# Kernel tuning notes

Measured on AMD Instinct MI355X. Metric: run time of the kernel, lower is better.

## Reference

```python
import jax, jax.numpy as jnp
import numpy as np

B, C, H, W = 4, 256, 64, 64
CQK = C // 2


def setup_inputs() -> dict:
    key = jax.random.key(0)
    ks = jax.random.split(key, 8)
    s = 0.05
    return {
        "x": jax.random.normal(ks[0], (B, C, H, W), dtype=jnp.float32),
        "wq": jax.random.normal(ks[1], (CQK, C), dtype=jnp.float32) * s,
        "bq": jax.random.normal(ks[2], (CQK,), dtype=jnp.float32) * s,
        "wk": jax.random.normal(ks[3], (CQK, C), dtype=jnp.float32) * s,
        "bk": jax.random.normal(ks[4], (CQK,), dtype=jnp.float32) * s,
        "wv": jax.random.normal(ks[5], (C, C), dtype=jnp.float32) * s,
        "bv": jax.random.normal(ks[6], (C,), dtype=jnp.float32) * s,
        "gamma": jax.random.normal(ks[7], (1,), dtype=jnp.float32),
    }


def reference(x, wq, bq, wk, bk, wv, bv, gamma):
    b, c, h, w = x.shape
    n = h * w
    xf = x.reshape(b, c, n)  # [B,C,N]
    # 1x1 convs == per-pixel linear projections
    q = jnp.einsum("oc,bcn->bon", wq, xf) + bq[:, None]  # [B,C/2,N]
    k = jnp.einsum("oc,bcn->bon", wk, xf) + bk[:, None]  # [B,C/2,N]
    v = jnp.einsum("oc,bcn->bon", wv, xf) + bv[:, None]  # [B,C,N]
    # attention[b,m,n'] = softmax_n'( sum_d q[b,d,m] * k[b,d,n'] )
    scores = jnp.einsum("bdm,bdn->bmn", q, k)  # [B,N,N]
    attn = jax.nn.softmax(scores, axis=2)
    # out_feat[b,c,j] = sum_i v[b,c,i] * attn[b,i,j]  (matmul(value, attention))
    af = jnp.einsum("bci,bij->bcj", v, attn)  # [B,C,N]
    out = gamma[0] * af.reshape(b, c, h, w) + x
    return out
```

## Files before the change

kernel.cpp:

```cpp
#include <hip/hip_runtime.h>
#include <hip/hip_bf16.h>


typedef _Float16 f16;
typedef _Float16 f16x4v __attribute__((ext_vector_type(4)));
typedef _Float16 f16x8v __attribute__((ext_vector_type(8)));
typedef float f32x4v __attribute__((ext_vector_type(4)));

static __device__ __forceinline__ f32x4v mfma16(f16x8v a, f16x8v b, f32x4v c) {
  return __builtin_amdgcn_mfma_f32_16x16x32_f16(a, b, c, 0, 0, 0);
}

__global__ void k_wcvt(const float* __restrict__ wq, const float* __restrict__ bq,
                       const float* __restrict__ wk, const float* __restrict__ bk,
                       const float* __restrict__ wv, const float* __restrict__ bv,
                       f16* __restrict__ wh, float* __restrict__ bcat) {
  int o = blockIdx.x;
  int c = threadIdx.x;
  const float* wrow; float bias;
  if (o < 128)      { wrow = wq + (size_t)o * 256;         bias = bq[o]; }
  else if (o < 256) { wrow = wk + (size_t)(o - 128) * 256; bias = bk[o - 128]; }
  else              { wrow = wv + (size_t)(o - 256) * 256; bias = bv[o - 256]; }
  wh[(size_t)(o >> 4) * 4096 + (size_t)(c >> 5) * 512 +
     (size_t)((c >> 3) & 3) * 128 + (o & 15) * 8 + (c & 7)] = (f16)wrow[c];
  if (c == 0) bcat[o] = bias;
}

__global__ void k_xsplit(const float* __restrict__ x, f16* __restrict__ xh) {
  __shared__ float t[64][65];
  int b = blockIdx.z, c0 = blockIdx.y * 64, n0 = blockIdx.x * 64;
  int tx = threadIdx.x & 63, ty = threadIdx.x >> 6;
  const float* xb = x + ((size_t)b * 256 + c0) * 4096 + n0;
#pragma unroll
  for (int r = ty; r < 64; r += 4) t[r][tx] = xb[(size_t)r * 4096 + tx];
  __syncthreads();
  f16* xbb = xh + (size_t)b * 1048576;
#pragma unroll
  for (int k2 = 0; k2 < 2; k2++) {
    int id = k2 * 256 + threadIdx.x;
    int tok = id & 63, oct = id >> 6;
    int tt = n0 + tok;
    f16x8v v;
#pragma unroll
    for (int e = 0; e < 8; e++) v[e] = (f16)t[oct * 8 + e][tok];
    size_t addr = (size_t)(tt >> 4) * 4096 +
                  (size_t)((c0 >> 5) + (oct >> 2)) * 512 +
                  (size_t)(oct & 3) * 128 + (tt & 15) * 8;
    *(f16x8v*)&xbb[addr] = v;
  }
}

__global__ void __launch_bounds__(512, 1)
k_proj(const f16* __restrict__ xh, const f16* __restrict__ wh,
       const float* __restrict__ bcat, f16* __restrict__ qT,
       f16* __restrict__ kT, f16* __restrict__ vT) {
  int ob = blockIdx.x, th = blockIdx.y, b = blockIdx.z;
  int tid = threadIdx.x, l = tid & 63, w = tid >> 6;
  int col = l & 15, quad = l >> 4;
  int tt = w & 3, oh = w >> 2;
  int OT0 = ob * 4 + oh * 2;
  const f16* wtb = wh + (size_t)OT0 * 4096 + l * 8;
  f16x8v wb[2][8];
#pragma unroll
  for (int jt = 0; jt < 2; jt++)
#pragma unroll
    for (int ks = 0; ks < 8; ks++)
      wb[jt][ks] = *(const f16x8v*)(wtb + jt * 4096 + ks * 512);
  float bias0 = bcat[OT0 * 16 + col];
  float bias1 = bcat[OT0 * 16 + 16 + col];
  const f16* atb = xh + (size_t)b * 1048576 + (size_t)(th * 32 + tt) * 4096 + l * 8;
  f16x8v afA[8], afB[8];
#pragma unroll
  for (int ks = 0; ks < 8; ks++) afA[ks] = *(const f16x8v*)(atb + ks * 512);

#define PROJ_BODY(IT, AF, AN, PREF)                                            \
  {                                                                            \
    if (PREF) {                                                                \
      _Pragma("unroll") for (int ks = 0; ks < 8; ks++)                         \
        AN[ks] = *(const f16x8v*)(atb + (size_t)((IT) + 1) * 16384 + ks * 512);\
    }                                                                          \
    f32x4v s0 = {}, s1 = {};                                                   \
    _Pragma("unroll") for (int ks = 0; ks < 8; ks++) {                         \
      s0 = mfma16(AF[ks], wb[0][ks], s0);                                      \
      s1 = mfma16(AF[ks], wb[1][ks], s1);                                      \
    }                                                                          \
    int T = th * 32 + (IT) * 4 + tt;                                           \
    if (ob < 4) {                                                              \
      f16* dst = (ob < 2) ? qT : kT;                                           \
      _Pragma("unroll") for (int jt = 0; jt < 2; jt++) {                       \
        int o = OT0 * 16 + jt * 16 + col;                                      \
        int d = o & 127;                                                       \
        float bs = jt ? bias1 : bias0;                                         \
        size_t base = (size_t)b * 524288 + (size_t)T * 2048 +                  \
                      (size_t)(d >> 5) * 512 + (size_t)((d >> 3) & 3) * 128 +  \
                      (d & 7);                                                 \
        float sv0 = jt ? s1[0] : s0[0], sv1 = jt ? s1[1] : s0[1];              \
        float sv2 = jt ? s1[2] : s0[2], sv3 = jt ? s1[3] : s0[3];              \
        dst[base + (quad * 4 + 0) * 8] = (f16)(sv0 + bs);                      \
        dst[base + (quad * 4 + 1) * 8] = (f16)(sv1 + bs);                      \
        dst[base + (quad * 4 + 2) * 8] = (f16)(sv2 + bs);                      \
        dst[base + (quad * 4 + 3) * 8] = (f16)(sv3 + bs);                      \
      }                                                                        \
    } else {                                                                   \
      int i0 = T * 16 + quad * 4;                                              \
      size_t ibase = (size_t)b * 1048576 + (size_t)(i0 >> 5) * 512 +           \
                     (size_t)((i0 >> 3) & 3) * 128 + (i0 & 7);                 \
      _Pragma("unroll") for (int jt = 0; jt < 2; jt++) {                       \
        int c = OT0 * 16 + jt * 16 + col - 256;                                \
        float bs = jt ? bias1 : bias0;                                         \
        f16x4v pv;                                                             \
        _Pragma("unroll") for (int rg = 0; rg < 4; rg++)                       \
          pv[rg] = (f16)((jt ? s1[rg] : s0[rg]) + bs);                         \
        *(f16x4v*)&vT[ibase + (size_t)(c >> 4) * 65536 + (c & 15) * 8] = pv;   \
      }                                                                        \
    }                                                                          \
  }

  for (int itp = 0; itp < 4; itp++) {
    int itA = itp * 2;
    PROJ_BODY(itA, afA, afB, true)
    PROJ_BODY(itA + 1, afB, afA, itp < 3)
  }
#undef PROJ_BODY
}

__global__ void __launch_bounds__(512, 2)
k_rows(const f16* __restrict__ qT, const f16* __restrict__ kT,
       float* __restrict__ partial) {
  int jblk = blockIdx.x, ih = blockIdx.y, b = blockIdx.z;
  int tid = threadIdx.x, l = tid & 63, w = tid >> 6;
  int col = l & 15;
  int ti = w & 3, jh = w >> 2;
  const f16* ktb = kT + (size_t)b * 524288 + (size_t)(jblk * 8 + jh * 4) * 2048 + l * 8;
  const f16* qtb = qT + (size_t)b * 524288 + (size_t)ti * 2048 + l * 8;
  f16x8v ka[4][4];
#pragma unroll
  for (int jt = 0; jt < 4; jt++)
#pragma unroll
    for (int ks = 0; ks < 4; ks++)
      ka[jt][ks] = *(const f16x8v*)(ktb + jt * 2048 + ks * 512);
  float* pout = partial + ((size_t)(b * 32 + jblk) * 2 + jh) * 4096 + ti * 16 + col;
  int it0 = ih * 16;
  f16x8v qfA[4], qfB[4];
#pragma unroll
  for (int ks = 0; ks < 4; ks++)
    qfA[ks] = *(const f16x8v*)(qtb + (size_t)it0 * 8192 + ks * 512);

#define ROWS_BODY(IT, QF, QN, PREF)                                           \
  {                                                                           \
    if (PREF) {                                                               \
      _Pragma("unroll") for (int ks = 0; ks < 4; ks++)                        \
        QN[ks] = *(const f16x8v*)(qtb + (size_t)((IT) + 1) * 8192 + ks * 512);\
    }                                                                         \
    f32x4v s[4] = {};                                                         \
    _Pragma("unroll") for (int ks = 0; ks < 4; ks++) {                        \
      s[0] = mfma16(ka[0][ks], QF[ks], s[0]);                                 \
      s[1] = mfma16(ka[1][ks], QF[ks], s[1]);                                 \
      s[2] = mfma16(ka[2][ks], QF[ks], s[2]);                                 \
      s[3] = mfma16(ka[3][ks], QF[ks], s[3]);                                 \
    }                                                                         \
    float t = 0.f;                                                            \
    _Pragma("unroll") for (int jt = 0; jt < 4; jt++)                          \
      _Pragma("unroll") for (int rg = 0; rg < 4; rg++)                        \
        t += __expf(s[jt][rg]);                                               \
    t += __shfl_xor(t, 16);                                                   \
    t += __shfl_xor(t, 32);                                                   \
    if (l < 16) pout[(size_t)(IT) * 64] = t;                                  \
  }

  for (int itp = 0; itp < 8; itp++) {
    int itA = it0 + itp * 2;
    ROWS_BODY(itA, qfA, qfB, true)
    ROWS_BODY(itA + 1, qfB, qfA, itp < 7)
  }
#undef ROWS_BODY
}

__global__ void k_rsum(const float* __restrict__ partial, float* __restrict__ rinv) {
  int b = blockIdx.y;
  int i = blockIdx.x * 256 + threadIdx.x;
  const float* p = partial + (size_t)b * 64 * 4096 + i;
  float s = 0.f;
#pragma unroll 8
  for (int jb = 0; jb < 64; jb++) s += p[(size_t)jb * 4096];
  rinv[(size_t)b * 4096 + i] = 1.0f / s;
}

__global__ void __launch_bounds__(512, 1)
k_fav(const f16* __restrict__ qT, const f16* __restrict__ kT,
      const f16* __restrict__ vT, const float* __restrict__ rinv,
      const float* __restrict__ x, const float* __restrict__ gamma,
      float* __restrict__ out) {
  __shared__ f16 sE[2][2][4096];
  int wg = blockIdx.x;
  int lg = (wg & 7) * 32 + (wg >> 3);
  int b = lg >> 6, j0 = (lg & 63) * 64;
  int tid = threadIdx.x, l = tid & 63, w = tid >> 6;
  int col = l & 15, quad = l >> 4;
  int ti = w & 3, tjb = (w >> 2) * 2;
  const f16* ktb = kT + (size_t)b * 524288 + (size_t)(j0 / 16 + tjb) * 2048 + l * 8;
  const f16* qtb = qT + (size_t)b * 524288 + (size_t)ti * 2048 + l * 8;
  const f16* vtb = vT + (size_t)b * 1048576 + (size_t)(w * 2) * 65536 + l * 8;
  const float* rp = rinv + (size_t)b * 4096 + ti * 16 + col;
  f16x8v ka0[4], ka1[4];
#pragma unroll
  for (int ks = 0; ks < 4; ks++) {
    ka0[ks] = *(const f16x8v*)(ktb + ks * 512);
    ka1[ks] = *(const f16x8v*)(ktb + 2048 + ks * 512);
  }
  f16x8v qfA[4], qfB[4], vfA[2][2], vfB[2][2];
  float rvA, rvB;
#pragma unroll
  for (int ks = 0; ks < 4; ks++) {
    qfA[ks] = *(const f16x8v*)(qtb + ks * 512);
    qfB[ks] = *(const f16x8v*)(qtb + 8192 + ks * 512);
  }
  rvA = rp[0];
  rvB = rp[64];
  f32x4v acc[2][4] = {};
  int ig = ti * 2 + (col >> 3);
  int i_lo = col & 7;

#define FAV_QK(QF, RV, SEP, SET)                                               \
  {                                                                            \
    f32x4v s0 = {}, s1 = {};                                                   \
    _Pragma("unroll") for (int ks = 0; ks < 4; ks++) {                         \
      s0 = mfma16(ka0[ks], QF[ks], s0);                                        \
      s1 = mfma16(ka1[ks], QF[ks], s1);                                        \
    }                                                                          \
    _Pragma("unroll") for (int rg = 0; rg < 4; rg++) {                         \
      int jl0 = tjb * 16 + quad * 4 + rg;                                      \
      sE[SEP][SET][jl0 * 64 + ((ig ^ (jl0 & 7)) * 8) + i_lo] =                 \
          (f16)(__expf(s0[rg]) * RV);                                          \
      sE[SEP][SET][(jl0 + 16) * 64 + ((ig ^ (jl0 & 7)) * 8) + i_lo] =          \
          (f16)(__expf(s1[rg]) * RV);                                          \
    }                                                                          \
  }

#define FAV_AV(VF, SEP, SET)                                                   \
  {                                                                            \
    _Pragma("unroll") for (int ks = 0; ks < 2; ks++) {                         \
      int sw = ((ks * 4 + quad) ^ (col & 7)) * 8;                              \
      f16x8v e0 = *(const f16x8v*)&sE[SEP][SET][col * 64 + sw];                \
      f16x8v e1 = *(const f16x8v*)&sE[SEP][SET][(16 + col) * 64 + sw];         \
      f16x8v e2 = *(const f16x8v*)&sE[SEP][SET][(32 + col) * 64 + sw];         \
      f16x8v e3 = *(const f16x8v*)&sE[SEP][SET][(48 + col) * 64 + sw];         \
      acc[0][0] = mfma16(VF[0][ks], e0, acc[0][0]);                            \
      acc[0][1] = mfma16(VF[0][ks], e1, acc[0][1]);                            \
      acc[0][2] = mfma16(VF[0][ks], e2, acc[0][2]);                            \
      acc[0][3] = mfma16(VF[0][ks], e3, acc[0][3]);                            \
      acc[1][0] = mfma16(VF[1][ks], e0, acc[1][0]);                            \
      acc[1][1] = mfma16(VF[1][ks], e1, acc[1][1]);                            \
      acc[1][2] = mfma16(VF[1][ks], e2, acc[1][2]);                            \
      acc[1][3] = mfma16(VF[1][ks], e3, acc[1][3]);                            \
    }                                                                          \
  }

  for (int s = 0; s < 32; s++) {
    int t0 = s * 2;
    int p = s & 1;
#pragma unroll
    for (int mt = 0; mt < 2; mt++)
#pragma unroll
      for (int ks = 0; ks < 2; ks++) {
        vfA[mt][ks] = *(const f16x8v*)(vtb + mt * 65536 + (size_t)(t0 * 2 + ks) * 512);
        vfB[mt][ks] = *(const f16x8v*)(vtb + mt * 65536 + (size_t)(t0 * 2 + 2 + ks) * 512);
      }
    if (p) { FAV_QK(qfA, rvA, 1, 0) FAV_QK(qfB, rvB, 1, 1) }
    else   { FAV_QK(qfA, rvA, 0, 0) FAV_QK(qfB, rvB, 0, 1) }
    asm volatile("s_waitcnt lgkmcnt(0)\n\ts_barrier" ::: "memory");
    if (s < 31) {
#pragma unroll
      for (int ks = 0; ks < 4; ks++) {
        qfA[ks] = *(const f16x8v*)(qtb + (size_t)(t0 + 2) * 8192 + ks * 512);
        qfB[ks] = *(const f16x8v*)(qtb + (size_t)(t0 + 3) * 8192 + ks * 512);
      }
      rvA = rp[(size_t)(t0 + 2) * 64];
      rvB = rp[(size_t)(t0 + 3) * 64];
    }
    if (p) { FAV_AV(vfA, 1, 0) FAV_AV(vfB, 1, 1) }
    else   { FAV_AV(vfA, 0, 0) FAV_AV(vfB, 0, 1) }
  }
#undef FAV_QK
#undef FAV_AV

  float gm = gamma[0];
  const float* xb = x + (size_t)b * 256 * 4096;
  float* ob = out + (size_t)b * 256 * 4096;
#pragma unroll
  for (int mt = 0; mt < 2; mt++)
#pragma unroll
    for (int jt = 0; jt < 4; jt++) {
      int c = w * 32 + mt * 16 + quad * 4;
      int j = j0 + jt * 16 + col;
#pragma unroll
      for (int rg = 0; rg < 4; rg++) {
        size_t off = (size_t)(c + rg) * 4096 + j;
        ob[off] = gm * acc[mt][jt][rg] + xb[off];
      }
    }
}

extern "C" void kernel_launch(void* const* d_in, const int* in_sizes, int n_in,
                              void* d_out, int out_size, void* d_ws, size_t ws_size,
                              hipStream_t stream) {
  (void)in_sizes; (void)n_in; (void)out_size; (void)ws_size;
  const float* x  = (const float*)d_in[0];
  const float* wq = (const float*)d_in[1];
  const float* bq = (const float*)d_in[2];
  const float* wk = (const float*)d_in[3];
  const float* bk = (const float*)d_in[4];
  const float* wv = (const float*)d_in[5];
  const float* bv = (const float*)d_in[6];
  const float* gm = (const float*)d_in[7];
  float* out = (float*)d_out;

  char* ws = (char*)d_ws;
  f16*  xh = (f16*)ws;
  f16*  qT = (f16*)(ws + 8388608);
  f16*  kT = (f16*)(ws + 12582912);
  f16*  vT = (f16*)(ws + 16777216);
  f16*  wh = (f16*)(ws + 25165824);
  float* bcat    = (float*)(ws + 25427968);
  float* rinv    = (float*)(ws + 25430016);
  float* partial = (float*)(ws + 25495552);

  hipLaunchKernelGGL(k_wcvt, dim3(512), dim3(256), 0, stream, wq, bq, wk, bk, wv, bv, wh, bcat);
  hipLaunchKernelGGL(k_xsplit, dim3(64, 4, 4), dim3(256), 0, stream, x, xh);
  hipLaunchKernelGGL(k_proj, dim3(8, 8, 4), dim3(512), 0, stream, xh, wh, bcat, qT, kT, vT);
  hipLaunchKernelGGL(k_rows, dim3(32, 4, 4), dim3(512), 0, stream, qT, kT, partial);
  hipLaunchKernelGGL(k_rsum, dim3(16, 4), dim3(256), 0, stream, partial, rinv);
  hipLaunchKernelGGL(k_fav, dim3(256), dim3(512), 0, stream, qT, kT, vT, rinv, x, gm, out);
}
```

Measured before the change: 180.9 us.

## Merge weight conversion into x split, halve row-sum grid, restructure fav QK split

Folds the weight/bias conversion kernel into the x transpose kernel, removing one launch. The row-sum kernel now processes twice as many query rows per block with half the grid, so each block's register-resident K fragments are reused over more rows. In the fused attention kernel, each wave now computes all four 16-column key tiles for one query tile rather than two key tiles for two query tiles. This cuts per-iteration Q loads and holds more K fragments in registers, at the cost of higher register pressure and a different mix of MFMA and LDS-write work.

```diff
diff --git a/kernel.cpp b/kernel.cpp
--- a/kernel.cpp
+++ b/kernel.cpp
@@ -11,22 +11,22 @@
   return __builtin_amdgcn_mfma_f32_16x16x32_f16(a, b, c, 0, 0, 0);
 }
 
-__global__ void k_wcvt(const float* __restrict__ wq, const float* __restrict__ bq,
-                       const float* __restrict__ wk, const float* __restrict__ bk,
-                       const float* __restrict__ wv, const float* __restrict__ bv,
-                       f16* __restrict__ wh, float* __restrict__ bcat) {
-  int o = blockIdx.x;
-  int c = threadIdx.x;
-  const float* wrow; float bias;
-  if (o < 128)      { wrow = wq + (size_t)o * 256;         bias = bq[o]; }
-  else if (o < 256) { wrow = wk + (size_t)(o - 128) * 256; bias = bk[o - 128]; }
-  else              { wrow = wv + (size_t)(o - 256) * 256; bias = bv[o - 256]; }
-  wh[(size_t)(o >> 4) * 4096 + (size_t)(c >> 5) * 512 +
-     (size_t)((c >> 3) & 3) * 128 + (o & 15) * 8 + (c & 7)] = (f16)wrow[c];
-  if (c == 0) bcat[o] = bias;
-}
-
-__global__ void k_xsplit(const float* __restrict__ x, f16* __restrict__ xh) {
+__global__ void k_xsplit(const float* __restrict__ x, f16* __restrict__ xh,
+                         const float* __restrict__ wq, const float* __restrict__ bq,
+                         const float* __restrict__ wk, const float* __restrict__ bk,
+                         const float* __restrict__ wv, const float* __restrict__ bv,
+                         f16* __restrict__ wh, float* __restrict__ bcat) {
+  int id = blockIdx.x + 64 * (blockIdx.y + 4 * blockIdx.z);
+  if (id < 512) {
+    int o = id, c = threadIdx.x;
+    const float* wrow; float bias;
+    if (o < 128)      { wrow = wq + (size_t)o * 256;         bias = bq[o]; }
+    else if (o < 256) { wrow = wk + (size_t)(o - 128) * 256; bias = bk[o - 128]; }
+    else              { wrow = wv + (size_t)(o - 256) * 256; bias = bv[o - 256]; }
+    wh[(size_t)(o >> 4) * 4096 + (size_t)(c >> 5) * 512 +
+       (size_t)((c >> 3) & 3) * 128 + (o & 15) * 8 + (c & 7)] = (f16)wrow[c];
+    if (c == 0) bcat[o] = bias;
+  }
   __shared__ float t[64][65];
   int b = blockIdx.z, c0 = blockIdx.y * 64, n0 = blockIdx.x * 64;
   int tx = threadIdx.x & 63, ty = threadIdx.x >> 6;
@@ -37,8 +37,8 @@
   f16* xbb = xh + (size_t)b * 1048576;
 #pragma unroll
   for (int k2 = 0; k2 < 2; k2++) {
-    int id = k2 * 256 + threadIdx.x;
-    int tok = id & 63, oct = id >> 6;
+    int id2 = k2 * 256 + threadIdx.x;
+    int tok = id2 & 63, oct = id2 >> 6;
     int tt = n0 + tok;
     f16x8v v;
 #pragma unroll
@@ -140,7 +140,7 @@
     for (int ks = 0; ks < 4; ks++)
       ka[jt][ks] = *(const f16x8v*)(ktb + jt * 2048 + ks * 512);
   float* pout = partial + ((size_t)(b * 32 + jblk) * 2 + jh) * 4096 + ti * 16 + col;
-  int it0 = ih * 16;
+  int it0 = ih * 32;
   f16x8v qfA[4], qfB[4];
 #pragma unroll
   for (int ks = 0; ks < 4; ks++)
@@ -168,10 +168,10 @@
     if (l < 16) pout[(size_t)(IT) * 64] = t;                                  \
   }
 
-  for (int itp = 0; itp < 8; itp++) {
+  for (int itp = 0; itp < 16; itp++) {
     int itA = it0 + itp * 2;
     ROWS_BODY(itA, qfA, qfB, true)
-    ROWS_BODY(itA + 1, qfB, qfA, itp < 7)
+    ROWS_BODY(itA + 1, qfB, qfA, itp < 15)
   }
 #undef ROWS_BODY
 }
@@ -197,54 +197,41 @@
   int b = lg >> 6, j0 = (lg & 63) * 64;
   int tid = threadIdx.x, l = tid & 63, w = tid >> 6;
   int col = l & 15, quad = l >> 4;
-  int ti = w & 3, tjb = (w >> 2) * 2;
-  const f16* ktb = kT + (size_t)b * 524288 + (size_t)(j0 / 16 + tjb) * 2048 + l * 8;
+  int ti = w & 3, sel = w >> 2;
+  const f16* ktb = kT + (size_t)b * 524288 + (size_t)(j0 / 16) * 2048 + l * 8;
   const f16* qtb = qT + (size_t)b * 524288 + (size_t)ti * 2048 + l * 8;
   const f16* vtb = vT + (size_t)b * 1048576 + (size_t)(w * 2) * 65536 + l * 8;
   const float* rp = rinv + (size_t)b * 4096 + ti * 16 + col;
-  f16x8v ka0[4], ka1[4];
-#pragma unroll
-  for (int ks = 0; ks < 4; ks++) {
-    ka0[ks] = *(const f16x8v*)(ktb + ks * 512);
-    ka1[ks] = *(const f16x8v*)(ktb + 2048 + ks * 512);
-  }
-  f16x8v qfA[4], qfB[4], vfA[2][2], vfB[2][2];
-  float rvA, rvB;
-#pragma unroll
-  for (int ks = 0; ks < 4; ks++) {
-    qfA[ks] = *(const f16x8v*)(qtb + ks * 512);
-    qfB[ks] = *(const f16x8v*)(qtb + 8192 + ks * 512);
-  }
-  rvA = rp[0];
-  rvB = rp[64];
+  f16x8v ka[4][4];
+#pragma unroll
+  for (int jt = 0; jt < 4; jt++)
+#pragma unroll
+    for (int ks = 0; ks < 4; ks++)
+      ka[jt][ks] = *(const f16x8v*)(ktb + jt * 2048 + ks * 512);
+  f16x8v qf[4], vfA[2][2], vfB[2][2];
+#pragma unroll
+  for (int ks = 0; ks < 4; ks++)
+    qf[ks] = *(const f16x8v*)(qtb + (size_t)sel * 8192 + ks * 512);
+  float rv = rp[sel * 64];
   f32x4v acc[2][4] = {};
   int ig = ti * 2 + (col >> 3);
   int i_lo = col & 7;
 
-#define FAV_QK(QF, RV, SEP, SET)                                               \
-  {                                                                            \
-    f32x4v s0 = {}, s1 = {};                                                   \
-    _Pragma("unroll") for (int ks = 0; ks < 4; ks++) {                         \
-      s0 = mfma16(ka0[ks], QF[ks], s0);                                        \
-      s1 = mfma16(ka1[ks], QF[ks], s1);                                        \
-    }                                                                          \
-    _Pragma("unroll") for (int rg = 0; rg < 4; rg++) {                         \
-      int jl0 = tjb * 16 + quad * 4 + rg;                                      \
-      sE[SEP][SET][jl0 * 64 + ((ig ^ (jl0 & 7)) * 8) + i_lo] =                 \
-          (f16)(__expf(s0[rg]) * RV);                                          \
-      sE[SEP][SET][(jl0 + 16) * 64 + ((ig ^ (jl0 & 7)) * 8) + i_lo] =          \
-          (f16)(__expf(s1[rg]) * RV);                                          \
-    }                                                                          \
-  }
-
-#define FAV_AV(VF, SEP, SET)                                                   \
+#define FAV_WR(SJ, JT, P)                                                      \
+  _Pragma("unroll") for (int rg = 0; rg < 4; rg++) {                           \
+    int jl = (JT) * 16 + quad * 4 + rg;                                        \
+    sE[P][sel][jl * 64 + ((ig ^ (jl & 7)) * 8) + i_lo] =                       \
+        (f16)(__expf(SJ[rg]) * rv);                                            \
+  }
+
+#define FAV_AV(VF, P, SET)                                                     \
   {                                                                            \
     _Pragma("unroll") for (int ks = 0; ks < 2; ks++) {                         \
       int sw = ((ks * 4 + quad) ^ (col & 7)) * 8;                              \
-      f16x8v e0 = *(const f16x8v*)&sE[SEP][SET][col * 64 + sw];                \
-      f16x8v e1 = *(const f16x8v*)&sE[SEP][SET][(16 + col) * 64 + sw];         \
-      f16x8v e2 = *(const f16x8v*)&sE[SEP][SET][(32 + col) * 64 + sw];         \
-      f16x8v e3 = *(const f16x8v*)&sE[SEP][SET][(48 + col) * 64 + sw];         \
+      f16x8v e0 = *(const f16x8v*)&sE[P][SET][col * 64 + sw];                  \
+      f16x8v e1 = *(const f16x8v*)&sE[P][SET][(16 + col) * 64 + sw];           \
+      f16x8v e2 = *(const f16x8v*)&sE[P][SET][(32 + col) * 64 + sw];           \
+      f16x8v e3 = *(const f16x8v*)&sE[P][SET][(48 + col) * 64 + sw];           \
       acc[0][0] = mfma16(VF[0][ks], e0, acc[0][0]);                            \
       acc[0][1] = mfma16(VF[0][ks], e1, acc[0][1]);                            \
       acc[0][2] = mfma16(VF[0][ks], e2, acc[0][2]);                            \
@@ -262,26 +249,34 @@
 #pragma unroll
     for (int mt = 0; mt < 2; mt++)
 #pragma unroll
-      for (int ks = 0; ks < 2; ks++) {
+      for (int ks = 0; ks < 2; ks++)
         vfA[mt][ks] = *(const f16x8v*)(vtb + mt * 65536 + (size_t)(t0 * 2 + ks) * 512);
+    f32x4v sj0 = {}, sj1 = {}, sj2 = {}, sj3 = {};
+#pragma unroll
+    for (int ks = 0; ks < 4; ks++) {
+      sj0 = mfma16(ka[0][ks], qf[ks], sj0);
+      sj1 = mfma16(ka[1][ks], qf[ks], sj1);
+      sj2 = mfma16(ka[2][ks], qf[ks], sj2);
+      sj3 = mfma16(ka[3][ks], qf[ks], sj3);
+    }
+#pragma unroll
+    for (int mt = 0; mt < 2; mt++)
+#pragma unroll
+      for (int ks = 0; ks < 2; ks++)
         vfB[mt][ks] = *(const f16x8v*)(vtb + mt * 65536 + (size_t)(t0 * 2 + 2 + ks) * 512);
-      }
-    if (p) { FAV_QK(qfA, rvA, 1, 0) FAV_QK(qfB, rvB, 1, 1) }
-    else   { FAV_QK(qfA, rvA, 0, 0) FAV_QK(qfB, rvB, 0, 1) }
+    if (p) { FAV_WR(sj0, 0, 1) FAV_WR(sj1, 1, 1) FAV_WR(sj2, 2, 1) FAV_WR(sj3, 3, 1) }
+    else   { FAV_WR(sj0, 0, 0) FAV_WR(sj1, 1, 0) FAV_WR(sj2, 2, 0) FAV_WR(sj3, 3, 0) }
     asm volatile("s_waitcnt lgkmcnt(0)\n\ts_barrier" ::: "memory");
     if (s < 31) {
 #pragma unroll
-      for (int ks = 0; ks < 4; ks++) {
-        qfA[ks] = *(const f16x8v*)(qtb + (size_t)(t0 + 2) * 8192 + ks * 512);
-        qfB[ks] = *(const f16x8v*)(qtb + (size_t)(t0 + 3) * 8192 + ks * 512);
-      }
-      rvA = rp[(size_t)(t0 + 2) * 64];
-      rvB = rp[(size_t)(t0 + 3) * 64];
+      for (int ks = 0; ks < 4; ks++)
+        qf[ks] = *(const f16x8v*)(qtb + (size_t)(t0 + 2 + sel) * 8192 + ks * 512);
+      rv = rp[(size_t)(t0 + 2 + sel) * 64];
     }
     if (p) { FAV_AV(vfA, 1, 0) FAV_AV(vfB, 1, 1) }
     else   { FAV_AV(vfA, 0, 0) FAV_AV(vfB, 0, 1) }
   }
-#undef FAV_QK
+#undef FAV_WR
 #undef FAV_AV
 
   float gm = gamma[0];
@@ -325,10 +320,10 @@
   float* rinv    = (float*)(ws + 25430016);
   float* partial = (float*)(ws + 25495552);
 
-  hipLaunchKernelGGL(k_wcvt, dim3(512), dim3(256), 0, stream, wq, bq, wk, bk, wv, bv, wh, bcat);
-  hipLaunchKernelGGL(k_xsplit, dim3(64, 4, 4), dim3(256), 0, stream, x, xh);
+  hipLaunchKernelGGL(k_xsplit, dim3(64, 4, 4), dim3(256), 0, stream,
+                     x, xh, wq, bq, wk, bk, wv, bv, wh, bcat);
   hipLaunchKernelGGL(k_proj, dim3(8, 8, 4), dim3(512), 0, stream, xh, wh, bcat, qT, kT, vT);
-  hipLaunchKernelGGL(k_rows, dim3(32, 4, 4), dim3(512), 0, stream, qT, kT, partial);
+  hipLaunchKernelGGL(k_rows, dim3(32, 2, 4), dim3(512), 0, stream, qT, kT, partial);
   hipLaunchKernelGGL(k_rsum, dim3(16, 4), dim3(256), 0, stream, partial, rinv);
   hipLaunchKernelGGL(k_fav, dim3(256), dim3(512), 0, stream, qT, kT, vT, rinv, x, gm, out);
 }
```

New measurement: 174.3 us. 1.04x faster.
